# Optimization experiments

Hardware: AMD Instinct MI355X
Metric: run time of the kernel (lower is better)

The kernel has to match this reference:

```python
import jax, jax.numpy as jnp
import numpy as np

DOWNSAMPLE = 512  # points per cloud, from init_kwargs


def _pairwise_dist(x, y):
    """Batched Euclidean distance matrix. x: (B,n,D), y: (B,m,D) -> (B,n,m)."""
    x2 = jnp.sum(x * x, axis=-1)                     # (B,n)
    y2 = jnp.sum(y * y, axis=-1)                     # (B,m)
    d2 = x2[:, :, None] + y2[:, None, :] - 2.0 * jnp.einsum('bnd,bmd->bnm', x, y)
    pos = d2 > 0.0                                   # guard sqrt(0)/negatives from fp error
    return jnp.where(pos, jnp.sqrt(jnp.where(pos, d2, 1.0)), 0.0)


def setup_inputs() -> dict:
    key = jax.random.key(0)
    k1, k2 = jax.random.split(key)
    inp = jax.random.normal(k1, (65536, 128), dtype=jnp.float32)
    tgt = jax.random.normal(k2, (65536, 128), dtype=jnp.float32)
    return {"input": inp, "target": tgt}


def reference(input, target):
    D = input.shape[-1]
    x = input.reshape(-1, DOWNSAMPLE, D)   # (B, n, D)
    y = target.reshape(-1, DOWNSAMPLE, D)  # (B, n, D)
    # geomloss energy kernel loss with uniform weights:
    # L_b = mean||x-y|| - 0.5*mean||x-x'|| - 0.5*mean||y-y'||
    cross = jnp.mean(_pairwise_dist(x, y), axis=(1, 2))  # (B,)
    xx = jnp.mean(_pairwise_dist(x, x), axis=(1, 2))
    yy = jnp.mean(_pairwise_dist(y, y), axis=(1, 2))
    loss = cross - 0.5 * xx - 0.5 * yy
    return jnp.mean(loss)
```

## Files before the change

kernel.cpp:

```cpp
#include <hip/hip_runtime.h>

typedef __attribute__((ext_vector_type(8))) __bf16 bf16x8;
typedef __attribute__((ext_vector_type(4))) float f32x4;
typedef __attribute__((ext_vector_type(8))) unsigned short ushort8;
typedef __attribute__((ext_vector_type(4))) unsigned short u16x4;

#define DSAMP 512
#define DIM   128
#define S1    ((size_t)16777216)
#define REG5  16384
#define NBPB  36
#define WS_NEEDED ((size_t)(4 * S1 + 2 * 262144 + 128 * NBPB * 4))

__global__ __launch_bounds__(256)
void presplit5(const float* __restrict__ x, const float* __restrict__ y,
               char* __restrict__ ws) {
    const size_t t = (size_t)blockIdx.x * 256 + threadIdx.x;
    const int jb = (int)(t & 7);
    const int c  = (int)((t >> 3) & 1);
    const int r  = (int)(t >> 4);
    const int input = r >> 16;
    const int ri    = r & 65535;

    const float* src = (input ? y : x) + ((size_t)ri << 7) + c * 64 + jb * 8;
    float4 v0 = ((const float4*)src)[0];
    float4 v1 = ((const float4*)src)[1];

    float s = v0.x * v0.x + v0.y * v0.y + v0.z * v0.z + v0.w * v0.w
            + v1.x * v1.x + v1.y * v1.y + v1.z * v1.z + v1.w * v1.w;
    #pragma unroll
    for (int o = 8; o > 0; o >>= 1) s += __shfl_down(s, o, 16);

    float xs[8] = {v0.x, v0.y, v0.z, v0.w, v1.x, v1.y, v1.z, v1.w};
    ushort8 hv, lv;
    #pragma unroll
    for (int e = 0; e < 8; ++e) {
        float xv = xs[e];
        unsigned ub = __float_as_uint(xv);
        unsigned hr = (ub + 0x7fffu + ((ub >> 16) & 1u)) >> 16;
        float hf = __uint_as_float(hr << 16);
        float rs = xv - hf;
        unsigned ul = __float_as_uint(rs);
        unsigned lr = (ul + 0x7fffu + ((ul >> 16) & 1u)) >> 16;
        hv[e] = (unsigned short)hr;
        lv[e] = (unsigned short)lr;
    }

    const int b  = ri >> 9;
    const int rb = ri & 511;
    char* hi = ws + (size_t)input * 2 * S1;
    char* lo = hi + S1;
    size_t off = ((size_t)(b * 2 + c) * 512 + rb) * 128
               + (size_t)((jb ^ (rb & 7)) * 16);
    *(ushort8*)(hi + off) = hv;
    *(ushort8*)(lo + off) = lv;

    if ((t & 15) == 0) {
        float* nG = (float*)(ws + 4 * S1) + (size_t)input * 65536;
        nG[ri] = s;
    }
}

__global__ __launch_bounds__(256, 3)
void mmd_tile7(const char* __restrict__ ws, float* __restrict__ partials) {
    __shared__ __align__(16) char smem[2 * REG5];
    __shared__ float Pn[128];
    __shared__ float Qn[128];
    __shared__ float wred[4];

    const int tid = threadIdx.x;
    const int xcd = blockIdx.x & 7;
    const int seq = blockIdx.x >> 3;
    const int b   = xcd + 8 * (seq / NBPB);
    const int s   = seq % NBPB;

    int type, ti, tj; float w; bool diag;
    if (s < 16) { type = 0; ti = s >> 2; tj = s & 3; w = 1.0f; diag = false; }
    else {
        int u = s - 16;
        type = 1 + (u >= 10);
        if (u >= 10) u -= 10;
        int i = (u >= 4) + (u >= 7) + (u >= 9);
        int off = (i == 1) ? 4 : (i == 2) ? 7 : (i == 3) ? 9 : 0;
        int j = u - off + i;
        ti = i; tj = j; diag = (i == j); w = diag ? -0.5f : -1.0f;
    }

    const char* Xhi = ws;
    const char* Yhi = ws + 2 * S1;
    const float* normX = (const float*)(ws + 4 * S1);
    const float* normY = normX + 65536;

    const char* Phi = (type == 2) ? Yhi : Xhi;
    const char* Qhi = (type == 1) ? Xhi : Yhi;
    const char* Qlo = Qhi + S1;
    const float* nP = (type == 2) ? normY : normX;
    const float* nQ = (type == 1) ? normX : normY;

    if (tid < 128) Pn[tid]       = nP[(size_t)b * 512 + ti * 128 + tid];
    else           Qn[tid - 128] = nQ[(size_t)b * 512 + tj * 128 + (tid - 128)];

    const int lane    = tid & 63;
    const int wv      = tid >> 6;
    const int rowHalf = (wv >> 1) * 64;
    const int colHalf = (wv & 1) * 64;
    const int fm      = lane & 15;
    const int kq      = lane >> 4;
    const int sw      = fm & 7;

    f32x4 acc[4][4];
    #pragma unroll
    for (int a2 = 0; a2 < 4; ++a2)
        #pragma unroll
        for (int b2 = 0; b2 < 4; ++b2)
            acc[a2][b2] = (f32x4){0.f, 0.f, 0.f, 0.f};

    for (int c = 0; c < 2; ++c) {
        if (c) __syncthreads();
        size_t chrow = (size_t)(b * 2 + c) * 512;
        {
            const char* srcs[2];
            srcs[0] = Phi + (chrow + (size_t)ti * 128) * 128;
            srcs[1] = Qhi + (chrow + (size_t)tj * 128) * 128;
            #pragma unroll
            for (int f = 0; f < 8; ++f) {
                int g = wv * 8 + f;
                int region = g >> 4;
                int sub    = g & 15;
                const char* gs = srcs[region] + sub * 1024 + lane * 16;
                char* ls = smem + (size_t)region * REG5 + sub * 1024 + lane * 16;
                __builtin_amdgcn_global_load_lds(
                    (const __attribute__((address_space(1))) void*)gs,
                    (__attribute__((address_space(3))) void*)ls, 16, 0, 0);
            }
        }
        bf16x8 bl[2][4];
        #pragma unroll
        for (int ks = 0; ks < 2; ++ks) {
            const int jx = ((ks * 4 + kq) ^ sw) * 16;
            #pragma unroll
            for (int b2 = 0; b2 < 4; ++b2) {
                size_t br = (size_t)(colHalf + b2 * 16 + fm);
                bl[ks][b2] = *(const bf16x8*)(Qlo + ((chrow + tj * 128 + br) << 7) + jx);
            }
        }
        __syncthreads();
        #pragma unroll
        for (int ks = 0; ks < 2; ++ks) {
            const int jx = ((ks * 4 + kq) ^ sw) * 16;
            bf16x8 ah[4], bh[4];
            #pragma unroll
            for (int a2 = 0; a2 < 4; ++a2) {
                int ar = rowHalf + a2 * 16 + fm;
                ah[a2] = *(const bf16x8*)(smem + ar * 128 + jx);
            }
            #pragma unroll
            for (int b2 = 0; b2 < 4; ++b2) {
                int br = colHalf + b2 * 16 + fm;
                bh[b2] = *(const bf16x8*)(smem + REG5 + br * 128 + jx);
            }
            #pragma unroll
            for (int a2 = 0; a2 < 4; ++a2)
                #pragma unroll
                for (int b2 = 0; b2 < 4; ++b2) {
                    acc[a2][b2] = __builtin_amdgcn_mfma_f32_16x16x32_bf16(ah[a2], bh[b2], acc[a2][b2], 0, 0, 0);
                    acc[a2][b2] = __builtin_amdgcn_mfma_f32_16x16x32_bf16(ah[a2], bl[ks][b2], acc[a2][b2], 0, 0, 0);
                }
        }
    }

    float Pr[16], Qc[4];
    #pragma unroll
    for (int a2 = 0; a2 < 4; ++a2)
        #pragma unroll
        for (int rg = 0; rg < 4; ++rg)
            Pr[a2 * 4 + rg] = Pn[rowHalf + a2 * 16 + kq * 4 + rg];
    #pragma unroll
    for (int b2 = 0; b2 < 4; ++b2) Qc[b2] = Qn[colHalf + b2 * 16 + fm];

    float lsum = 0.f;
    #pragma unroll
    for (int a2 = 0; a2 < 4; ++a2) {
        #pragma unroll
        for (int b2 = 0; b2 < 4; ++b2) {
            #pragma unroll
            for (int rg = 0; rg < 4; ++rg) {
                float d2 = fmaf(-2.0f, acc[a2][b2][rg], Pr[a2 * 4 + rg] + Qc[b2]);
                float v  = __builtin_amdgcn_sqrtf(fmaxf(d2, 0.0f));
                if (diag && (rowHalf + a2 * 16 + kq * 4 + rg) == (colHalf + b2 * 16 + fm))
                    v = 0.f;
                lsum += v;
            }
        }
    }
    #pragma unroll
    for (int off = 32; off > 0; off >>= 1) lsum += __shfl_down(lsum, off, 64);
    if (lane == 0) wred[wv] = lsum;
    __syncthreads();
    if (tid == 0)
        partials[blockIdx.x] = (wred[0] + wred[1] + wred[2] + wred[3]) * w;
}

__global__ __launch_bounds__(256, 2)
void mmd_tile_fallback(const float* __restrict__ x, const float* __restrict__ y,
                       float* __restrict__ partials) {
    __shared__ __align__(16) char smem[4 * 128 * 144];
    __shared__ float Pn[128];
    __shared__ float Qn[128];
    __shared__ float wred[4];

    char* Ah = smem;
    char* Al = smem + 1 * 128 * 144;
    char* Bh = smem + 2 * 128 * 144;
    char* Bl = smem + 3 * 128 * 144;

    const int tid  = threadIdx.x;
    const int bid  = blockIdx.x;
    const int tj   = bid & 3;
    const int ti   = (bid >> 2) & 3;
    const int type = (bid >> 4) % 3;
    const int b    = bid / 48;

    const float* Xb = x + (size_t)b * DSAMP * DIM;
    const float* Yb = y + (size_t)b * DSAMP * DIM;
    const float* Pp; const float* Qp; float w;
    if (type == 0)      { Pp = Xb; Qp = Yb; w = 1.0f;  }
    else if (type == 1) { Pp = Xb; Qp = Xb; w = -0.5f; }
    else                { Pp = Yb; Qp = Yb; w = -0.5f; }
    Pp += (size_t)ti * 128 * DIM;
    Qp += (size_t)tj * 128 * DIM;

    {
        const float* rp = (tid < 128) ? (Pp + (size_t)tid * DIM)
                                      : (Qp + (size_t)(tid - 128) * DIM);
        float s = 0.f;
        #pragma unroll
        for (int k4 = 0; k4 < 32; ++k4) {
            float4 v = ((const float4*)rp)[k4];
            s += v.x * v.x + v.y * v.y + v.z * v.z + v.w * v.w;
        }
        if (tid < 128) Pn[tid] = s; else Qn[tid - 128] = s;
    }

    const int lane    = tid & 63;
    const int wv      = tid >> 6;
    const int rowHalf = (wv >> 1) * 64;
    const int colHalf = (wv & 1) * 64;
    const int fm      = lane & 15;
    const int kq      = lane >> 4;

    f32x4 acc[4][4];
    #pragma unroll
    for (int a2 = 0; a2 < 4; ++a2)
        #pragma unroll
        for (int b2 = 0; b2 < 4; ++b2)
            acc[a2][b2] = (f32x4){0.f, 0.f, 0.f, 0.f};

    for (int c = 0; c < 2; ++c) {
        if (c) __syncthreads();
        #pragma unroll
        for (int side = 0; side < 2; ++side) {
            const float* sp = side ? Qp : Pp;
            char* dh = side ? Bh : Ah;
            char* dl = side ? Bl : Al;
            #pragma unroll
            for (int it = 0; it < 4; ++it) {
                int u  = it * 256 + tid;
                int r  = u >> 3;
                int c8 = u & 7;
                const float* g = sp + (size_t)r * DIM + c * 64 + c8 * 8;
                float4 v0 = ((const float4*)g)[0];
                float4 v1 = ((const float4*)g)[1];
                float xs[8] = {v0.x, v0.y, v0.z, v0.w, v1.x, v1.y, v1.z, v1.w};
                ushort8 hv, lv;
                #pragma unroll
                for (int e = 0; e < 8; ++e) {
                    float xv = xs[e];
                    unsigned ub = __float_as_uint(xv);
                    unsigned hr = (ub + 0x7fffu + ((ub >> 16) & 1u)) >> 16;
                    float hf = __uint_as_float(hr << 16);
                    float rs = xv - hf;
                    unsigned ul = __float_as_uint(rs);
                    unsigned lr = (ul + 0x7fffu + ((ul >> 16) & 1u)) >> 16;
                    hv[e] = (unsigned short)hr;
                    lv[e] = (unsigned short)lr;
                }
                *(ushort8*)(dh + r * 144 + c8 * 16) = hv;
                *(ushort8*)(dl + r * 144 + c8 * 16) = lv;
            }
        }
        __syncthreads();
        #pragma unroll
        for (int ks = 0; ks < 2; ++ks) {
            const int kb2 = (ks * 32 + kq * 8) * 2;
            bf16x8 ah[4], al[4], bh[4], bl[4];
            #pragma unroll
            for (int a2 = 0; a2 < 4; ++a2) {
                int ar = rowHalf + a2 * 16 + fm;
                ah[a2] = *(const bf16x8*)(Ah + ar * 144 + kb2);
                al[a2] = *(const bf16x8*)(Al + ar * 144 + kb2);
            }
            #pragma unroll
            for (int b2 = 0; b2 < 4; ++b2) {
                int br = colHalf + b2 * 16 + fm;
                bh[b2] = *(const bf16x8*)(Bh + br * 144 + kb2);
                bl[b2] = *(const bf16x8*)(Bl + br * 144 + kb2);
            }
            #pragma unroll
            for (int a2 = 0; a2 < 4; ++a2)
                #pragma unroll
                for (int b2 = 0; b2 < 4; ++b2) {
                    acc[a2][b2] = __builtin_amdgcn_mfma_f32_16x16x32_bf16(ah[a2], bh[b2], acc[a2][b2], 0, 0, 0);
                    acc[a2][b2] = __builtin_amdgcn_mfma_f32_16x16x32_bf16(ah[a2], bl[b2], acc[a2][b2], 0, 0, 0);
                    acc[a2][b2] = __builtin_amdgcn_mfma_f32_16x16x32_bf16(al[a2], bh[b2], acc[a2][b2], 0, 0, 0);
                }
        }
    }

    const bool selfm = (type != 0) && (ti == tj);
    float lsum = 0.f;
    #pragma unroll
    for (int a2 = 0; a2 < 4; ++a2) {
        int ib = rowHalf + a2 * 16 + kq * 4;
        #pragma unroll
        for (int b2 = 0; b2 < 4; ++b2) {
            int j = colHalf + b2 * 16 + fm;
            float qn = Qn[j];
            #pragma unroll
            for (int rg = 0; rg < 4; ++rg) {
                int i = ib + rg;
                float d2 = Pn[i] + qn - 2.0f * acc[a2][b2][rg];
                if (d2 > 0.f && !(selfm && i == j)) lsum += sqrtf(d2);
            }
        }
    }
    #pragma unroll
    for (int off = 32; off > 0; off >>= 1) lsum += __shfl_down(lsum, off, 64);
    if (lane == 0) wred[wv] = lsum;
    __syncthreads();
    if (tid == 0)
        partials[bid] = (wred[0] + wred[1] + wred[2] + wred[3]) * w;
}

__global__ __launch_bounds__(256)
void mmd_finalize_kernel(const float* __restrict__ partials, int n,
                         float* __restrict__ out, double scale) {
    __shared__ double sh[256];
    double s = 0.0;
    for (int i = threadIdx.x; i < n; i += 256) s += (double)partials[i];
    sh[threadIdx.x] = s;
    __syncthreads();
    for (int off = 128; off > 0; off >>= 1) {
        if ((int)threadIdx.x < off) sh[threadIdx.x] += sh[threadIdx.x + off];
        __syncthreads();
    }
    if (threadIdx.x == 0) out[0] = (float)(sh[0] * scale);
}

extern "C" void kernel_launch(void* const* d_in, const int* in_sizes, int n_in,
                              void* d_out, int out_size, void* d_ws, size_t ws_size,
                              hipStream_t stream) {
    const float* x = (const float*)d_in[0];
    const float* y = (const float*)d_in[1];
    float* out = (float*)d_out;

    const int n = in_sizes[0];
    const int B = n / (DSAMP * DIM);
    const double scale = 1.0 / ((double)B * (double)DSAMP * (double)DSAMP);

    if (ws_size >= WS_NEEDED) {
        char* ws = (char*)d_ws;
        float* partials = (float*)(ws + 4 * S1 + 2 * 262144);
        const int nthreads = (2 * n) / 8;
        const int nblocks = B * NBPB;
        presplit5<<<dim3(nthreads / 256), dim3(256), 0, stream>>>(x, y, ws);
        mmd_tile7<<<dim3(nblocks), dim3(256), 0, stream>>>(ws, partials);
        mmd_finalize_kernel<<<dim3(1), dim3(256), 0, stream>>>(partials, nblocks, out, scale);
    } else {
        float* partials = (float*)d_ws;
        const int nblocks = B * 48;
        mmd_tile_fallback<<<dim3(nblocks), dim3(256), 0, stream>>>(x, y, partials);
        mmd_finalize_kernel<<<dim3(1), dim3(256), 0, stream>>>(partials, nblocks, out, scale);
    }
}
```

Measured before the change: 147.7 us.

## Load both K-chunks into LDS at once, removing mid-loop barrier

The tile kernel now stages both 64-wide K chunks of P and Q into a doubled 64KB LDS buffer with a single batch of async global-to-LDS loads, and preloads all lo-part Q fragments up front. This drops the second load phase and its barrier, so memory latency is exposed once instead of twice. The epilogue is split into separate diagonal and non-diagonal paths, removing the per-element diagonal check from most tiles. In exchange LDS use and register pressure rise, and the occupancy hint drops from 3 to 2 blocks per CU.

```diff
diff --git a/kernel.cpp b/kernel.cpp
--- a/kernel.cpp
+++ b/kernel.cpp
@@ -61,9 +61,9 @@
     }
 }
 
-__global__ __launch_bounds__(256, 3)
-void mmd_tile7(const char* __restrict__ ws, float* __restrict__ partials) {
-    __shared__ __align__(16) char smem[2 * REG5];
+__global__ __launch_bounds__(256, 2)
+void mmd_tile8(const char* __restrict__ ws, float* __restrict__ partials) {
+    __shared__ __align__(16) char smem[4 * REG5];
     __shared__ float Pn[128];
     __shared__ float Qn[128];
     __shared__ float wred[4];
@@ -108,6 +108,35 @@
     const int kq      = lane >> 4;
     const int sw      = fm & 7;
 
+    {
+        const int c = wv & 1;
+        const int rr = (wv < 2) ? ti : tj;
+        const char* base = ((wv < 2) ? Phi : Qhi)
+                         + ((size_t)(b * 2 + c) * 512 + (size_t)rr * 128) * 128
+                         + (size_t)lane * 16;
+        char* ls = smem + (size_t)wv * REG5 + lane * 16;
+        #pragma unroll
+        for (int sub = 0; sub < 16; ++sub) {
+            __builtin_amdgcn_global_load_lds(
+                (const __attribute__((address_space(1))) void*)(base + sub * 1024),
+                (__attribute__((address_space(3))) void*)(ls + sub * 1024), 16, 0, 0);
+        }
+    }
+
+    bf16x8 bl[4][4];
+    #pragma unroll
+    for (int t = 0; t < 4; ++t) {
+        const int c  = t >> 1;
+        const int ks = t & 1;
+        const int jx = ((ks * 4 + kq) ^ sw) * 16;
+        const size_t rowbase = (size_t)(b * 2 + c) * 512 + (size_t)tj * 128;
+        #pragma unroll
+        for (int b2 = 0; b2 < 4; ++b2) {
+            size_t br = (size_t)(colHalf + b2 * 16 + fm);
+            bl[t][b2] = *(const bf16x8*)(Qlo + ((rowbase + br) << 7) + jx);
+        }
+    }
+
     f32x4 acc[4][4];
     #pragma unroll
     for (int a2 = 0; a2 < 4; ++a2)
@@ -115,58 +144,31 @@
         for (int b2 = 0; b2 < 4; ++b2)
             acc[a2][b2] = (f32x4){0.f, 0.f, 0.f, 0.f};
 
-    for (int c = 0; c < 2; ++c) {
-        if (c) __syncthreads();
-        size_t chrow = (size_t)(b * 2 + c) * 512;
-        {
-            const char* srcs[2];
-            srcs[0] = Phi + (chrow + (size_t)ti * 128) * 128;
-            srcs[1] = Qhi + (chrow + (size_t)tj * 128) * 128;
-            #pragma unroll
-            for (int f = 0; f < 8; ++f) {
-                int g = wv * 8 + f;
-                int region = g >> 4;
-                int sub    = g & 15;
-                const char* gs = srcs[region] + sub * 1024 + lane * 16;
-                char* ls = smem + (size_t)region * REG5 + sub * 1024 + lane * 16;
-                __builtin_amdgcn_global_load_lds(
-                    (const __attribute__((address_space(1))) void*)gs,
-                    (__attribute__((address_space(3))) void*)ls, 16, 0, 0);
-            }
-        }
-        bf16x8 bl[2][4];
-        #pragma unroll
-        for (int ks = 0; ks < 2; ++ks) {
-            const int jx = ((ks * 4 + kq) ^ sw) * 16;
+    __syncthreads();
+
+    #pragma unroll
+    for (int t = 0; t < 4; ++t) {
+        const int c  = t >> 1;
+        const int ks = t & 1;
+        const int jx = ((ks * 4 + kq) ^ sw) * 16;
+        bf16x8 ah[4], bh[4];
+        #pragma unroll
+        for (int a2 = 0; a2 < 4; ++a2) {
+            int ar = rowHalf + a2 * 16 + fm;
+            ah[a2] = *(const bf16x8*)(smem + (size_t)c * REG5 + ar * 128 + jx);
+        }
+        #pragma unroll
+        for (int b2 = 0; b2 < 4; ++b2) {
+            int br = colHalf + b2 * 16 + fm;
+            bh[b2] = *(const bf16x8*)(smem + (size_t)(2 + c) * REG5 + br * 128 + jx);
+        }
+        #pragma unroll
+        for (int a2 = 0; a2 < 4; ++a2)
             #pragma unroll
             for (int b2 = 0; b2 < 4; ++b2) {
-                size_t br = (size_t)(colHalf + b2 * 16 + fm);
-                bl[ks][b2] = *(const bf16x8*)(Qlo + ((chrow + tj * 128 + br) << 7) + jx);
-            }
-        }
-        __syncthreads();
-        #pragma unroll
-        for (int ks = 0; ks < 2; ++ks) {
-            const int jx = ((ks * 4 + kq) ^ sw) * 16;
-            bf16x8 ah[4], bh[4];
-            #pragma unroll
-            for (int a2 = 0; a2 < 4; ++a2) {
-                int ar = rowHalf + a2 * 16 + fm;
-                ah[a2] = *(const bf16x8*)(smem + ar * 128 + jx);
-            }
-            #pragma unroll
-            for (int b2 = 0; b2 < 4; ++b2) {
-                int br = colHalf + b2 * 16 + fm;
-                bh[b2] = *(const bf16x8*)(smem + REG5 + br * 128 + jx);
-            }
-            #pragma unroll
-            for (int a2 = 0; a2 < 4; ++a2)
-                #pragma unroll
-                for (int b2 = 0; b2 < 4; ++b2) {
-                    acc[a2][b2] = __builtin_amdgcn_mfma_f32_16x16x32_bf16(ah[a2], bh[b2], acc[a2][b2], 0, 0, 0);
-                    acc[a2][b2] = __builtin_amdgcn_mfma_f32_16x16x32_bf16(ah[a2], bl[ks][b2], acc[a2][b2], 0, 0, 0);
-                }
-        }
+                acc[a2][b2] = __builtin_amdgcn_mfma_f32_16x16x32_bf16(ah[a2], bh[b2], acc[a2][b2], 0, 0, 0);
+                acc[a2][b2] = __builtin_amdgcn_mfma_f32_16x16x32_bf16(ah[a2], bl[t][b2], acc[a2][b2], 0, 0, 0);
+            }
     }
 
     float Pr[16], Qc[4];
@@ -179,19 +181,29 @@
     for (int b2 = 0; b2 < 4; ++b2) Qc[b2] = Qn[colHalf + b2 * 16 + fm];
 
     float lsum = 0.f;
-    #pragma unroll
-    for (int a2 = 0; a2 < 4; ++a2) {
-        #pragma unroll
-        for (int b2 = 0; b2 < 4; ++b2) {
-            #pragma unroll
-            for (int rg = 0; rg < 4; ++rg) {
-                float d2 = fmaf(-2.0f, acc[a2][b2][rg], Pr[a2 * 4 + rg] + Qc[b2]);
-                float v  = __builtin_amdgcn_sqrtf(fmaxf(d2, 0.0f));
-                if (diag && (rowHalf + a2 * 16 + kq * 4 + rg) == (colHalf + b2 * 16 + fm))
-                    v = 0.f;
-                lsum += v;
-            }
-        }
+    if (diag) {
+        #pragma unroll
+        for (int a2 = 0; a2 < 4; ++a2)
+            #pragma unroll
+            for (int b2 = 0; b2 < 4; ++b2)
+                #pragma unroll
+                for (int rg = 0; rg < 4; ++rg) {
+                    float d2 = fmaf(-2.0f, acc[a2][b2][rg], Pr[a2 * 4 + rg] + Qc[b2]);
+                    float v  = __builtin_amdgcn_sqrtf(fmaxf(d2, 0.0f));
+                    if ((rowHalf + a2 * 16 + kq * 4 + rg) == (colHalf + b2 * 16 + fm))
+                        v = 0.f;
+                    lsum += v;
+                }
+    } else {
+        #pragma unroll
+        for (int a2 = 0; a2 < 4; ++a2)
+            #pragma unroll
+            for (int b2 = 0; b2 < 4; ++b2)
+                #pragma unroll
+                for (int rg = 0; rg < 4; ++rg) {
+                    float d2 = fmaf(-2.0f, acc[a2][b2][rg], Pr[a2 * 4 + rg] + Qc[b2]);
+                    lsum += __builtin_amdgcn_sqrtf(fmaxf(d2, 0.0f));
+                }
     }
     #pragma unroll
     for (int off = 32; off > 0; off >>= 1) lsum += __shfl_down(lsum, off, 64);
@@ -374,7 +386,7 @@
         const int nthreads = (2 * n) / 8;
         const int nblocks = B * NBPB;
         presplit5<<<dim3(nthreads / 256), dim3(256), 0, stream>>>(x, y, ws);
-        mmd_tile7<<<dim3(nblocks), dim3(256), 0, stream>>>(ws, partials);
+        mmd_tile8<<<dim3(nblocks), dim3(256), 0, stream>>>(ws, partials);
         mmd_finalize_kernel<<<dim3(1), dim3(256), 0, stream>>>(partials, nblocks, out, scale);
     } else {
         float* partials = (float*)d_ws;
```

New measurement: 151.5 us. 2.5% more time.
